# Optimization experiments

Measured on AMD Instinct MI355X. Metric: run time of the kernel, lower is better.

Reference implementation:

```python
import jax, jax.numpy as jnp
import numpy as np

N = 100000
E = 1600000
G = 64  # number of graphs
H = 128
BN_EPS = 1e-5


def setup_inputs() -> dict:
    key = jax.random.key(0)
    ks = jax.random.split(key, 12)
    x = jax.random.normal(ks[0], (N, 3), dtype=jnp.float32)
    edge_index = jax.random.randint(ks[1], (2, E), 0, N, dtype=jnp.int64)
    batch = jnp.sort(jax.random.randint(ks[2], (N,), 0, G, dtype=jnp.int64))
    W1 = jax.random.normal(ks[3], (3, H), dtype=jnp.float32) * 0.3
    W2 = jax.random.normal(ks[4], (H, H), dtype=jnp.float32) * 0.05
    W3 = jax.random.normal(ks[5], (H, H), dtype=jnp.float32) * 0.05
    lin_W = jax.random.normal(ks[6], (H, 2), dtype=jnp.float32) * 0.05
    d = {
        'x': x, 'edge_index': edge_index, 'batch': batch,
        'W1': W1, 'b1': jnp.zeros((H,), jnp.float32),
        'W2': W2, 'b2': jnp.zeros((H,), jnp.float32),
        'W3': W3, 'b3': jnp.zeros((H,), jnp.float32),
        'lin_W': lin_W, 'lin_b': jnp.zeros((2,), jnp.float32),
    }
    for i, kk in zip((1, 2, 3), ks[7:10]):
        d[f'bn{i}_g'] = jnp.ones((H,), jnp.float32)
        d[f'bn{i}_b'] = jnp.zeros((H,), jnp.float32)
        d[f'bn{i}_m'] = jnp.zeros((H,), jnp.float32)
        d[f'bn{i}_v'] = jax.random.uniform(kk, (H,), dtype=jnp.float32, minval=0.5, maxval=1.5)
    return d


def _gcn(x, src, dst, norm, W, b):
    # GCNConv: out = scatter_add(norm * (xW)[src], dst) + b
    h = x @ W
    msg = h[src] * norm[:, None]
    agg = jax.ops.segment_sum(msg, dst, num_segments=N)
    return agg + b


def _bn_eval(x, g, b, m, v):
    return (x - m) * jax.lax.rsqrt(v + BN_EPS) * g + b


def reference(x, edge_index, batch, W1, b1, W2, b2, W3, b3,
              bn1_g, bn1_b, bn1_m, bn1_v,
              bn2_g, bn2_b, bn2_m, bn2_v,
              bn3_g, bn3_b, bn3_m, bn3_v,
              lin_W, lin_b):
    loop = jnp.arange(N, dtype=edge_index.dtype)
    src = jnp.concatenate([edge_index[0], loop])
    dst = jnp.concatenate([edge_index[1], loop])
    # symmetric normalization with self-loops: deg from destination nodes
    deg = jax.ops.segment_sum(jnp.ones_like(dst, dtype=x.dtype), dst, num_segments=N)
    dinv = jnp.where(deg > 0, jax.lax.rsqrt(deg), 0.0)
    norm = dinv[src] * dinv[dst]

    h = jax.nn.relu(_bn_eval(_gcn(x, src, dst, norm, W1, b1), bn1_g, bn1_b, bn1_m, bn1_v))
    h = jax.nn.relu(_bn_eval(_gcn(h, src, dst, norm, W2, b2), bn2_g, bn2_b, bn2_m, bn2_v))
    h = jax.nn.relu(_bn_eval(_gcn(h, src, dst, norm, W3, b3), bn3_g, bn3_b, bn3_m, bn3_v))
    # dropout is identity in eval mode
    sums = jax.ops.segment_sum(h, batch, num_segments=G)
    cnts = jax.ops.segment_sum(jnp.ones((N,), h.dtype), batch, num_segments=G)
    pooled = sums / jnp.maximum(cnts, 1.0)[:, None]
    return pooled @ lin_W + lin_b
```

## Files before the change

kernel.cpp:

```cpp
#include <hip/hip_runtime.h>

#define NN 100000
#define EE 1600000
#define GG 64
#define HH 128
#define BN_EPS 1e-5f

#define CB 782
#define NB 256
#define TILE 6250

typedef unsigned short ushort_t;

static __device__ inline ushort_t f2bf(float f) {
    unsigned u = __float_as_uint(f);
    unsigned r = (u + 0x7FFF + ((u >> 16) & 1)) >> 16;
    return (ushort_t)r;
}
static __device__ inline float bf2f(ushort_t b) {
    return __uint_as_float(((unsigned)b) << 16);
}


__global__ __launch_bounds__(256) void k_hist(const int* __restrict__ ei,
                                              int* __restrict__ histG) {
    __shared__ int h[CB];
    int t = threadIdx.x;
    for (int i = t; i < CB; i += 256) h[i] = 0;
    __syncthreads();
    int e0 = blockIdx.x * TILE;
    for (int i = t; i < TILE; i += 256) {
        int d = ei[EE + e0 + i];
        atomicAdd(&h[d >> 7], 1);
    }
    __syncthreads();
    for (int i = t; i < CB; i += 256) histG[blockIdx.x * CB + i] = h[i];
}

__global__ __launch_bounds__(NB) void k_bscan(int* __restrict__ histG,
                                              int* __restrict__ total) {
    __shared__ int sh[NB];
    int t = threadIdx.x;
    int c = blockIdx.x;
    sh[t] = histG[t * CB + c];
    __syncthreads();
    for (int d = 1; d < NB; d <<= 1) {
        int x = (t >= d) ? sh[t - d] : 0;
        __syncthreads();
        sh[t] += x;
        __syncthreads();
    }
    histG[t * CB + c] = (t > 0) ? sh[t - 1] : 0;
    if (t == NB - 1) total[c] = sh[NB - 1];
}

__global__ __launch_bounds__(1024) void k_cbase(const int* __restrict__ total,
                                                int* __restrict__ cbase) {
    __shared__ int sh[1024];
    int t = threadIdx.x;
    sh[t] = (t < CB) ? total[t] : 0;
    __syncthreads();
    for (int d = 1; d < 1024; d <<= 1) {
        int x = (t >= d) ? sh[t - d] : 0;
        __syncthreads();
        sh[t] += x;
        __syncthreads();
    }
    if (t < CB) cbase[t] = (t > 0) ? sh[t - 1] : 0;
    if (t == CB - 1) cbase[CB] = sh[t];
}

__global__ __launch_bounds__(256) void k_cscatter(const int* __restrict__ ei,
                                                  const int* __restrict__ histG,
                                                  const int* __restrict__ cbase,
                                                  int* __restrict__ metaS) {
    __shared__ int base_l[CB];
    __shared__ int cur_l[CB];
    int t = threadIdx.x;
    int b = blockIdx.x;
    for (int i = t; i < CB; i += 256) {
        base_l[i] = cbase[i] + histG[b * CB + i];
        cur_l[i] = 0;
    }
    __syncthreads();
    int e0 = b * TILE;
    for (int i = t; i < TILE; i += 256) {
        int s = ei[e0 + i];
        int d = ei[EE + e0 + i];
        int c = d >> 7;
        int p = base_l[c] + atomicAdd(&cur_l[c], 1);
        metaS[p] = s | ((d & 127) << 17);
    }
}

__global__ __launch_bounds__(256) void k_fine(const int* __restrict__ metaS,
                                              const int* __restrict__ cbase,
                                              int* __restrict__ cnt,
                                              int* __restrict__ offs,
                                              int* __restrict__ col,
                                              float* __restrict__ dinv) {
    __shared__ int hist[128];
    __shared__ int scn[128];
    __shared__ int cur[128];
    int t = threadIdx.x;
    int c = blockIdx.x;
    int lo = cbase[c], hi = cbase[c + 1];
    if (t < 128) hist[t] = 0;
    __syncthreads();
    for (int r = lo + t; r < hi; r += 256) atomicAdd(&hist[metaS[r] >> 17], 1);
    __syncthreads();
    if (t < 128) scn[t] = hist[t];
    __syncthreads();
    for (int d = 1; d < 128; d <<= 1) {
        int x = (t >= d && t < 128) ? scn[t - d] : 0;
        __syncthreads();
        if (t < 128) scn[t] += x;
        __syncthreads();
    }
    if (t < 128) {
        int excl = (t > 0) ? scn[t - 1] : 0;
        cur[t] = excl;
        int node = c * 128 + t;
        if (node < NN) {
            cnt[node] = hist[t];
            offs[node] = lo + excl;
            dinv[node] = rsqrtf((float)(hist[t] + 1));
        }
    }
    __syncthreads();
    for (int r = lo + t; r < hi; r += 256) {
        int pk = metaS[r];
        int s = pk & 0x1FFFF;
        int idx = atomicAdd(&cur[pk >> 17], 1);
        col[lo + idx] = s;
    }
}


__global__ __launch_bounds__(256) void k_aggx(const float* __restrict__ x,
                                              const int* __restrict__ offs,
                                              const int* __restrict__ cnt,
                                              const int* __restrict__ col,
                                              const float* __restrict__ dinv,
                                              float* __restrict__ wgt,
                                              float4* __restrict__ agg) {
    int tid = threadIdx.x;
    int wave = tid >> 6;
    int lane = tid & 63;
    int grp = lane >> 4;
    int l = lane & 15;
    int n = blockIdx.x * 16 + wave * 4 + grp;
    float dv = dinv[n];
    int base = offs[n], cn = cnt[n];
    float a0 = 0.f, a1 = 0.f, a2 = 0.f;
    for (int i = l; i < cn; i += 16) {
        int s = col[base + i];
        float w = dinv[s] * dv;
        wgt[base + i] = w;
        a0 += w * x[s * 3 + 0];
        a1 += w * x[s * 3 + 1];
        a2 += w * x[s * 3 + 2];
    }
#pragma unroll
    for (int off = 8; off >= 1; off >>= 1) {
        a0 += __shfl_xor(a0, off, 16);
        a1 += __shfl_xor(a1, off, 16);
        a2 += __shfl_xor(a2, off, 16);
    }
    if (l == 0) {
        float w0 = dv * dv;
        a0 += w0 * x[n * 3 + 0];
        a1 += w0 * x[n * 3 + 1];
        a2 += w0 * x[n * 3 + 2];
        agg[n] = make_float4(a0, a1, a2, 0.f);
    }
}


__global__ __launch_bounds__(256) void k_mml1(const float4* __restrict__ agg,
                                              const float* __restrict__ W1,
                                              const float* __restrict__ b1,
                                              const float* __restrict__ g1,
                                              const float* __restrict__ bb1,
                                              const float* __restrict__ m1,
                                              const float* __restrict__ v1,
                                              const float* __restrict__ W2,
                                              ushort_t* __restrict__ outB) {
    __shared__ float xs[64][132];
    __shared__ float4 ag[64];
    int tid = threadIdx.x;
    int row0 = blockIdx.x * 64;
    if (tid < 64) {
        int gr = row0 + tid;
        ag[tid] = (gr < NN) ? agg[gr] : make_float4(0.f, 0.f, 0.f, 0.f);
    }
    __syncthreads();
    {
        int c = tid & 127;
        int rh = tid >> 7;
        float w0 = W1[c], w1 = W1[128 + c], w2 = W1[256 + c];
        float sc = g1[c] * rsqrtf(v1[c] + BN_EPS);
        float sh = (b1[c] - m1[c]) * sc + bb1[c];
#pragma unroll
        for (int i = 0; i < 32; i++) {
            int r = 2 * i + rh;
            float4 a = ag[r];
            float t = a.x * w0 + a.y * w1 + a.z * w2;
            xs[r][c] = fmaxf(t * sc + sh, 0.f);
        }
    }
    __syncthreads();

    int tx = tid & 31;
    int ty = tid >> 5;
    float acc[8][4];
#pragma unroll
    for (int i = 0; i < 8; i++)
#pragma unroll
        for (int j = 0; j < 4; j++) acc[i][j] = 0.f;

    const float* Wp = W2 + tx * 4;
#pragma unroll 4
    for (int k = 0; k < 128; k++) {
        float4 w = *(const float4*)&Wp[k * HH];
#pragma unroll
        for (int i = 0; i < 8; i++) {
            float xv = xs[ty * 8 + i][k];
            acc[i][0] += xv * w.x;
            acc[i][1] += xv * w.y;
            acc[i][2] += xv * w.z;
            acc[i][3] += xv * w.w;
        }
    }
#pragma unroll
    for (int i = 0; i < 8; i++) {
        int gr = row0 + ty * 8 + i;
        if (gr < NN) {
            ushort4 o;
            o.x = f2bf(acc[i][0]);
            o.y = f2bf(acc[i][1]);
            o.z = f2bf(acc[i][2]);
            o.w = f2bf(acc[i][3]);
            *(ushort4*)&outB[(size_t)gr * HH + tx * 4] = o;
        }
    }
}


__global__ __launch_bounds__(256) void k_mm(const ushort_t* __restrict__ xin,
                                            const float* __restrict__ W,
                                            ushort_t* __restrict__ outB) {
    __shared__ float xs[64][132];
    int tid = threadIdx.x;
    int tx = tid & 31;
    int ty = tid >> 5;
    int row0 = blockIdx.x * 64;
#pragma unroll
    for (int i = 0; i < 4; i++) {
        int idx8 = i * 256 + tid;
        int r = idx8 >> 4;
        int k8 = (idx8 & 15) * 8;
        int gr = row0 + r;
        int4 pk = (gr < NN) ? *(const int4*)&xin[(size_t)gr * HH + k8]
                            : make_int4(0, 0, 0, 0);
        float* dst = &xs[r][k8];
        dst[0] = __uint_as_float(((unsigned)pk.x) << 16);
        dst[1] = __uint_as_float(((unsigned)pk.x) & 0xFFFF0000u);
        dst[2] = __uint_as_float(((unsigned)pk.y) << 16);
        dst[3] = __uint_as_float(((unsigned)pk.y) & 0xFFFF0000u);
        dst[4] = __uint_as_float(((unsigned)pk.z) << 16);
        dst[5] = __uint_as_float(((unsigned)pk.z) & 0xFFFF0000u);
        dst[6] = __uint_as_float(((unsigned)pk.w) << 16);
        dst[7] = __uint_as_float(((unsigned)pk.w) & 0xFFFF0000u);
    }
    __syncthreads();
    float acc[8][4];
#pragma unroll
    for (int i = 0; i < 8; i++)
#pragma unroll
        for (int j = 0; j < 4; j++) acc[i][j] = 0.f;

    const float* Wp = W + tx * 4;
#pragma unroll 4
    for (int k = 0; k < 128; k++) {
        float4 w = *(const float4*)&Wp[k * HH];
#pragma unroll
        for (int i = 0; i < 8; i++) {
            float xv = xs[ty * 8 + i][k];
            acc[i][0] += xv * w.x;
            acc[i][1] += xv * w.y;
            acc[i][2] += xv * w.z;
            acc[i][3] += xv * w.w;
        }
    }
#pragma unroll
    for (int i = 0; i < 8; i++) {
        int gr = row0 + ty * 8 + i;
        if (gr < NN) {
            ushort4 o;
            o.x = f2bf(acc[i][0]);
            o.y = f2bf(acc[i][1]);
            o.z = f2bf(acc[i][2]);
            o.w = f2bf(acc[i][3]);
            *(ushort4*)&outB[(size_t)gr * HH + tx * 4] = o;
        }
    }
}


__global__ __launch_bounds__(256) void k_agg(const ushort_t* __restrict__ t,
                                             const int* __restrict__ offs,
                                             const int* __restrict__ cnt,
                                             const int* __restrict__ col,
                                             const float* __restrict__ wgt,
                                             const float* __restrict__ dinv,
                                             const float* __restrict__ bias,
                                             const float* __restrict__ g,
                                             const float* __restrict__ bb,
                                             const float* __restrict__ m,
                                             const float* __restrict__ v,
                                             ushort_t* __restrict__ out) {
    int wave = threadIdx.x >> 6;
    int lane = threadIdx.x & 63;
    int half = lane >> 5;
    int l = lane & 31;
    int d = blockIdx.x * 8 + wave * 2 + half;
    int c0 = l * 4;
    float dv = dinv[d];
    float w0 = dv * dv;
    ushort4 selfR = *(const ushort4*)&t[(size_t)d * HH + c0];
    float4 acc;
    acc.x = bf2f(selfR.x) * w0; acc.y = bf2f(selfR.y) * w0;
    acc.z = bf2f(selfR.z) * w0; acc.w = bf2f(selfR.w) * w0;
    int base = offs[d], cn = cnt[d];
    for (int ib = 0; ib < cn; ib += 32) {
        int i = ib + l;
        int s = 0;
        float w = 0.f;
        if (i < cn) {
            s = col[base + i];
            w = wgt[base + i];
        }
        int lim = min(32, cn - ib);
#pragma unroll 8
        for (int j = 0; j < lim; j++) {
            int ss = __shfl(s, j, 32);
            float ww = __shfl(w, j, 32);
            ushort4 tv = *(const ushort4*)&t[(size_t)ss * HH + c0];
            acc.x += ww * bf2f(tv.x);
            acc.y += ww * bf2f(tv.y);
            acc.z += ww * bf2f(tv.z);
            acc.w += ww * bf2f(tv.w);
        }
    }
    float4 gg = *(const float4*)&g[c0];
    float4 vv = *(const float4*)&v[c0];
    float4 mm = *(const float4*)&m[c0];
    float4 bv = *(const float4*)&bb[c0];
    float4 bi = *(const float4*)&bias[c0];
    float sc0 = gg.x * rsqrtf(vv.x + BN_EPS);
    float sc1 = gg.y * rsqrtf(vv.y + BN_EPS);
    float sc2 = gg.z * rsqrtf(vv.z + BN_EPS);
    float sc3 = gg.w * rsqrtf(vv.w + BN_EPS);
    ushort4 o;
    o.x = f2bf(fmaxf(acc.x * sc0 + (bi.x - mm.x) * sc0 + bv.x, 0.f));
    o.y = f2bf(fmaxf(acc.y * sc1 + (bi.y - mm.y) * sc1 + bv.y, 0.f));
    o.z = f2bf(fmaxf(acc.z * sc2 + (bi.z - mm.z) * sc2 + bv.z, 0.f));
    o.w = f2bf(fmaxf(acc.w * sc3 + (bi.w - mm.w) * sc3 + bv.w, 0.f));
    *(ushort4*)&out[(size_t)d * HH + c0] = o;
}


#define PBLK 2048
__global__ void k_pool(const ushort_t* __restrict__ h, const int* __restrict__ batch,
                       float* __restrict__ gsum, int* __restrict__ gcnt) {
    int c = threadIdx.x;
    int per = (NN + PBLK - 1) / PBLK;
    int n0 = blockIdx.x * per;
    int n1 = min(NN, n0 + per);
    if (n0 >= NN) return;
    float acc = 0.f;
    int cur = batch[n0];
    int count = 0;
    for (int n = n0; n < n1; n++) {
        int gr = batch[n];
        if (gr != cur) {
            atomicAdd(&gsum[cur * HH + c], acc);
            if (c == 0) atomicAdd(&gcnt[cur], count);
            acc = 0.f; count = 0; cur = gr;
        }
        acc += bf2f(h[(size_t)n * HH + c]);
        count++;
    }
    atomicAdd(&gsum[cur * HH + c], acc);
    if (c == 0) atomicAdd(&gcnt[cur], count);
}

__global__ void k_head(const float* __restrict__ gsum, const int* __restrict__ gcnt,
                       const float* __restrict__ linW, const float* __restrict__ linb,
                       float* __restrict__ out) {
    int t = threadIdx.x;
    int gr = t >> 1, j = t & 1;
    float inv = 1.0f / fmaxf((float)gcnt[gr], 1.0f);
    float acc = 0.f;
    for (int c = 0; c < HH; c++) acc += gsum[gr * HH + c] * linW[c * 2 + j];
    out[t] = acc * inv + linb[j];
}


static inline size_t al256(size_t x) { return (x + 255) & ~(size_t)255; }

extern "C" void kernel_launch(void* const* d_in, const int* in_sizes, int n_in,
                              void* d_out, int out_size, void* d_ws, size_t ws_size,
                              hipStream_t stream) {
    const float* x    = (const float*)d_in[0];
    const int*   ei   = (const int*)d_in[1];
    const int*   batch= (const int*)d_in[2];
    const float* W1   = (const float*)d_in[3];
    const float* b1   = (const float*)d_in[4];
    const float* W2   = (const float*)d_in[5];
    const float* b2   = (const float*)d_in[6];
    const float* W3   = (const float*)d_in[7];
    const float* b3   = (const float*)d_in[8];
    const float* linW = (const float*)d_in[9];
    const float* linb = (const float*)d_in[10];
    const float* bn1g = (const float*)d_in[11];
    const float* bn1b = (const float*)d_in[12];
    const float* bn1m = (const float*)d_in[13];
    const float* bn1v = (const float*)d_in[14];
    const float* bn2g = (const float*)d_in[15];
    const float* bn2b = (const float*)d_in[16];
    const float* bn2m = (const float*)d_in[17];
    const float* bn2v = (const float*)d_in[18];
    const float* bn3g = (const float*)d_in[19];
    const float* bn3b = (const float*)d_in[20];
    const float* bn3m = (const float*)d_in[21];
    const float* bn3v = (const float*)d_in[22];
    float* out = (float*)d_out;

    char* ws = (char*)d_ws;
    size_t off = 0;
    int*    histG  = (int*)(ws + off);    off += al256((size_t)NB * CB * 4);
    int*    total  = (int*)(ws + off);    off += al256((size_t)CB * 4);
    int*    cbase  = (int*)(ws + off);    off += al256((size_t)(CB + 1) * 4);
    int*    cnt    = (int*)(ws + off);    off += al256((size_t)NN * 4);
    int*    offs   = (int*)(ws + off);    off += al256((size_t)NN * 4);
    float*  dinv   = (float*)(ws + off);  off += al256((size_t)NN * 4);
    int*    col    = (int*)(ws + off);    off += al256((size_t)EE * 4);
    float*  wgt    = (float*)(ws + off);  off += al256((size_t)EE * 4);
    float4* agg    = (float4*)(ws + off); off += al256((size_t)NN * 16);
    char*   bufA   = (char*)(ws + off);   off += al256((size_t)NN * HH * 2);
    char*   bufB   = (char*)(ws + off);   off += al256((size_t)NN * HH * 4);
    float*  gsum   = (float*)(ws + off);  off += (size_t)GG * HH * 4;
    int*    gcnt   = (int*)(ws + off);    off += al256((size_t)GG * 4);

    int* metaS = (int*)bufB;
    ushort_t* tB = (ushort_t*)bufB;
    ushort_t* hB = (ushort_t*)bufA;

    hipMemsetAsync(gsum, 0, (size_t)GG * HH * 4 + (size_t)GG * 4, stream);

    k_hist<<<NB, 256, 0, stream>>>(ei, histG);
    k_bscan<<<CB, NB, 0, stream>>>(histG, total);
    k_cbase<<<1, 1024, 0, stream>>>(total, cbase);
    k_cscatter<<<NB, 256, 0, stream>>>(ei, histG, cbase, metaS);
    k_fine<<<CB, 256, 0, stream>>>(metaS, cbase, cnt, offs, col, dinv);

    k_aggx<<<NN / 16, 256, 0, stream>>>(x, offs, cnt, col, dinv, wgt, agg);

    k_mml1<<<(NN + 63) / 64, 256, 0, stream>>>(agg, W1, b1, bn1g, bn1b, bn1m, bn1v,
                                               W2, tB);
    k_agg<<<NN / 8, 256, 0, stream>>>(tB, offs, cnt, col, wgt, dinv,
                                      b2, bn2g, bn2b, bn2m, bn2v, hB);

    k_mm<<<(NN + 63) / 64, 256, 0, stream>>>(hB, W3, tB);
    k_agg<<<NN / 8, 256, 0, stream>>>(tB, offs, cnt, col, wgt, dinv,
                                      b3, bn3g, bn3b, bn3m, bn3v, hB);

    k_pool<<<PBLK, 128, 0, stream>>>(hB, batch, gsum, gcnt);
    k_head<<<1, 128, 0, stream>>>(gsum, gcnt, linW, linb, out);
}
```

Measured before the change: 442.8 us.

## Fuse GCN aggregation with following matmul and pooling into per-tile kernels

Merges the layer-1 x aggregation into the first matmul kernel, fuses layer-2 aggregation+BN+ReLU with the layer-3 matmul through shared memory, and fuses layer-3 aggregation with mean pooling. The per-edge weight array is no longer stored; weights are recomputed from dinv on the fly. This removes intermediate bf16 activation round-trips to global memory and several kernel launches. The cost is lower parallelism per block (64 nodes per block, fewer blocks) and a larger block size for the fused aggregation kernels.

```diff
diff --git a/kernel.cpp b/kernel.cpp
--- a/kernel.cpp
+++ b/kernel.cpp
@@ -137,62 +137,55 @@
 }
 
 
-__global__ __launch_bounds__(256) void k_aggx(const float* __restrict__ x,
-                                              const int* __restrict__ offs,
-                                              const int* __restrict__ cnt,
-                                              const int* __restrict__ col,
-                                              const float* __restrict__ dinv,
-                                              float* __restrict__ wgt,
-                                              float4* __restrict__ agg) {
-    int tid = threadIdx.x;
-    int wave = tid >> 6;
-    int lane = tid & 63;
-    int grp = lane >> 4;
-    int l = lane & 15;
-    int n = blockIdx.x * 16 + wave * 4 + grp;
-    float dv = dinv[n];
-    int base = offs[n], cn = cnt[n];
-    float a0 = 0.f, a1 = 0.f, a2 = 0.f;
-    for (int i = l; i < cn; i += 16) {
-        int s = col[base + i];
-        float w = dinv[s] * dv;
-        wgt[base + i] = w;
-        a0 += w * x[s * 3 + 0];
-        a1 += w * x[s * 3 + 1];
-        a2 += w * x[s * 3 + 2];
-    }
-#pragma unroll
-    for (int off = 8; off >= 1; off >>= 1) {
-        a0 += __shfl_xor(a0, off, 16);
-        a1 += __shfl_xor(a1, off, 16);
-        a2 += __shfl_xor(a2, off, 16);
-    }
-    if (l == 0) {
-        float w0 = dv * dv;
-        a0 += w0 * x[n * 3 + 0];
-        a1 += w0 * x[n * 3 + 1];
-        a2 += w0 * x[n * 3 + 2];
-        agg[n] = make_float4(a0, a1, a2, 0.f);
-    }
-}
-
-
-__global__ __launch_bounds__(256) void k_mml1(const float4* __restrict__ agg,
-                                              const float* __restrict__ W1,
-                                              const float* __restrict__ b1,
-                                              const float* __restrict__ g1,
-                                              const float* __restrict__ bb1,
-                                              const float* __restrict__ m1,
-                                              const float* __restrict__ v1,
-                                              const float* __restrict__ W2,
-                                              ushort_t* __restrict__ outB) {
+__global__ __launch_bounds__(256) void k_l12(const float* __restrict__ x,
+                                             const int* __restrict__ offs,
+                                             const int* __restrict__ cnt,
+                                             const int* __restrict__ col,
+                                             const float* __restrict__ dinv,
+                                             const float* __restrict__ W1,
+                                             const float* __restrict__ b1,
+                                             const float* __restrict__ g1,
+                                             const float* __restrict__ bb1,
+                                             const float* __restrict__ m1,
+                                             const float* __restrict__ v1,
+                                             const float* __restrict__ W2,
+                                             ushort_t* __restrict__ outB) {
     __shared__ float xs[64][132];
     __shared__ float4 ag[64];
     int tid = threadIdx.x;
     int row0 = blockIdx.x * 64;
-    if (tid < 64) {
-        int gr = row0 + tid;
-        ag[tid] = (gr < NN) ? agg[gr] : make_float4(0.f, 0.f, 0.f, 0.f);
+    int hw = tid >> 5;
+    int l = tid & 31;
+    for (int k = 0; k < 8; k++) {
+        int r = hw * 8 + k;
+        int d = row0 + r;
+        float a0 = 0.f, a1 = 0.f, a2 = 0.f;
+        if (d < NN) {
+            float dv = dinv[d];
+            int base = offs[d], cn2 = cnt[d];
+            for (int i = l; i < cn2; i += 32) {
+                int s = col[base + i];
+                float w = dinv[s] * dv;
+                a0 += w * x[s * 3 + 0];
+                a1 += w * x[s * 3 + 1];
+                a2 += w * x[s * 3 + 2];
+            }
+#pragma unroll
+            for (int off = 16; off >= 1; off >>= 1) {
+                a0 += __shfl_xor(a0, off, 32);
+                a1 += __shfl_xor(a1, off, 32);
+                a2 += __shfl_xor(a2, off, 32);
+            }
+            if (l == 0) {
+                float w0 = dv * dv;
+                a0 += w0 * x[d * 3 + 0];
+                a1 += w0 * x[d * 3 + 1];
+                a2 += w0 * x[d * 3 + 2];
+                ag[r] = make_float4(a0, a1, a2, 0.f);
+            }
+        } else if (l == 0) {
+            ag[r] = make_float4(0.f, 0.f, 0.f, 0.f);
+        }
     }
     __syncthreads();
     {
@@ -210,7 +203,6 @@
         }
     }
     __syncthreads();
-
     int tx = tid & 31;
     int ty = tid >> 5;
     float acc[8][4];
@@ -218,7 +210,6 @@
     for (int i = 0; i < 8; i++)
 #pragma unroll
         for (int j = 0; j < 4; j++) acc[i][j] = 0.f;
-
     const float* Wp = W2 + tx * 4;
 #pragma unroll 4
     for (int k = 0; k < 128; k++) {
@@ -247,112 +238,24 @@
 }
 
 
-__global__ __launch_bounds__(256) void k_mm(const ushort_t* __restrict__ xin,
-                                            const float* __restrict__ W,
-                                            ushort_t* __restrict__ outB) {
+__global__ __launch_bounds__(512) void k_aggmm(const ushort_t* __restrict__ t,
+                                               const int* __restrict__ offs,
+                                               const int* __restrict__ cnt,
+                                               const int* __restrict__ col,
+                                               const float* __restrict__ dinv,
+                                               const float* __restrict__ bias,
+                                               const float* __restrict__ g,
+                                               const float* __restrict__ bb,
+                                               const float* __restrict__ m,
+                                               const float* __restrict__ v,
+                                               const float* __restrict__ W3,
+                                               ushort_t* __restrict__ outB) {
     __shared__ float xs[64][132];
     int tid = threadIdx.x;
-    int tx = tid & 31;
-    int ty = tid >> 5;
     int row0 = blockIdx.x * 64;
-#pragma unroll
-    for (int i = 0; i < 4; i++) {
-        int idx8 = i * 256 + tid;
-        int r = idx8 >> 4;
-        int k8 = (idx8 & 15) * 8;
-        int gr = row0 + r;
-        int4 pk = (gr < NN) ? *(const int4*)&xin[(size_t)gr * HH + k8]
-                            : make_int4(0, 0, 0, 0);
-        float* dst = &xs[r][k8];
-        dst[0] = __uint_as_float(((unsigned)pk.x) << 16);
-        dst[1] = __uint_as_float(((unsigned)pk.x) & 0xFFFF0000u);
-        dst[2] = __uint_as_float(((unsigned)pk.y) << 16);
-        dst[3] = __uint_as_float(((unsigned)pk.y) & 0xFFFF0000u);
-        dst[4] = __uint_as_float(((unsigned)pk.z) << 16);
-        dst[5] = __uint_as_float(((unsigned)pk.z) & 0xFFFF0000u);
-        dst[6] = __uint_as_float(((unsigned)pk.w) << 16);
-        dst[7] = __uint_as_float(((unsigned)pk.w) & 0xFFFF0000u);
-    }
-    __syncthreads();
-    float acc[8][4];
-#pragma unroll
-    for (int i = 0; i < 8; i++)
-#pragma unroll
-        for (int j = 0; j < 4; j++) acc[i][j] = 0.f;
-
-    const float* Wp = W + tx * 4;
-#pragma unroll 4
-    for (int k = 0; k < 128; k++) {
-        float4 w = *(const float4*)&Wp[k * HH];
-#pragma unroll
-        for (int i = 0; i < 8; i++) {
-            float xv = xs[ty * 8 + i][k];
-            acc[i][0] += xv * w.x;
-            acc[i][1] += xv * w.y;
-            acc[i][2] += xv * w.z;
-            acc[i][3] += xv * w.w;
-        }
-    }
-#pragma unroll
-    for (int i = 0; i < 8; i++) {
-        int gr = row0 + ty * 8 + i;
-        if (gr < NN) {
-            ushort4 o;
-            o.x = f2bf(acc[i][0]);
-            o.y = f2bf(acc[i][1]);
-            o.z = f2bf(acc[i][2]);
-            o.w = f2bf(acc[i][3]);
-            *(ushort4*)&outB[(size_t)gr * HH + tx * 4] = o;
-        }
-    }
-}
-
-
-__global__ __launch_bounds__(256) void k_agg(const ushort_t* __restrict__ t,
-                                             const int* __restrict__ offs,
-                                             const int* __restrict__ cnt,
-                                             const int* __restrict__ col,
-                                             const float* __restrict__ wgt,
-                                             const float* __restrict__ dinv,
-                                             const float* __restrict__ bias,
-                                             const float* __restrict__ g,
-                                             const float* __restrict__ bb,
-                                             const float* __restrict__ m,
-                                             const float* __restrict__ v,
-                                             ushort_t* __restrict__ out) {
-    int wave = threadIdx.x >> 6;
-    int lane = threadIdx.x & 63;
-    int half = lane >> 5;
-    int l = lane & 31;
-    int d = blockIdx.x * 8 + wave * 2 + half;
+    int hw = tid >> 5;
+    int l = tid & 31;
     int c0 = l * 4;
-    float dv = dinv[d];
-    float w0 = dv * dv;
-    ushort4 selfR = *(const ushort4*)&t[(size_t)d * HH + c0];
-    float4 acc;
-    acc.x = bf2f(selfR.x) * w0; acc.y = bf2f(selfR.y) * w0;
-    acc.z = bf2f(selfR.z) * w0; acc.w = bf2f(selfR.w) * w0;
-    int base = offs[d], cn = cnt[d];
-    for (int ib = 0; ib < cn; ib += 32) {
-        int i = ib + l;
-        int s = 0;
-        float w = 0.f;
-        if (i < cn) {
-            s = col[base + i];
-            w = wgt[base + i];
-        }
-        int lim = min(32, cn - ib);
-#pragma unroll 8
-        for (int j = 0; j < lim; j++) {
-            int ss = __shfl(s, j, 32);
-            float ww = __shfl(w, j, 32);
-            ushort4 tv = *(const ushort4*)&t[(size_t)ss * HH + c0];
-            acc.x += ww * bf2f(tv.x);
-            acc.y += ww * bf2f(tv.y);
-            acc.z += ww * bf2f(tv.z);
-            acc.w += ww * bf2f(tv.w);
-        }
-    }
     float4 gg = *(const float4*)&g[c0];
     float4 vv = *(const float4*)&v[c0];
     float4 mm = *(const float4*)&m[c0];
@@ -362,38 +265,190 @@
     float sc1 = gg.y * rsqrtf(vv.y + BN_EPS);
     float sc2 = gg.z * rsqrtf(vv.z + BN_EPS);
     float sc3 = gg.w * rsqrtf(vv.w + BN_EPS);
-    ushort4 o;
-    o.x = f2bf(fmaxf(acc.x * sc0 + (bi.x - mm.x) * sc0 + bv.x, 0.f));
-    o.y = f2bf(fmaxf(acc.y * sc1 + (bi.y - mm.y) * sc1 + bv.y, 0.f));
-    o.z = f2bf(fmaxf(acc.z * sc2 + (bi.z - mm.z) * sc2 + bv.z, 0.f));
-    o.w = f2bf(fmaxf(acc.w * sc3 + (bi.w - mm.w) * sc3 + bv.w, 0.f));
-    *(ushort4*)&out[(size_t)d * HH + c0] = o;
-}
-
-
-#define PBLK 2048
-__global__ void k_pool(const ushort_t* __restrict__ h, const int* __restrict__ batch,
-                       float* __restrict__ gsum, int* __restrict__ gcnt) {
-    int c = threadIdx.x;
-    int per = (NN + PBLK - 1) / PBLK;
-    int n0 = blockIdx.x * per;
-    int n1 = min(NN, n0 + per);
-    if (n0 >= NN) return;
-    float acc = 0.f;
-    int cur = batch[n0];
-    int count = 0;
-    for (int n = n0; n < n1; n++) {
-        int gr = batch[n];
-        if (gr != cur) {
-            atomicAdd(&gsum[cur * HH + c], acc);
-            if (c == 0) atomicAdd(&gcnt[cur], count);
-            acc = 0.f; count = 0; cur = gr;
-        }
-        acc += bf2f(h[(size_t)n * HH + c]);
-        count++;
-    }
-    atomicAdd(&gsum[cur * HH + c], acc);
-    if (c == 0) atomicAdd(&gcnt[cur], count);
+    float sh0 = (bi.x - mm.x) * sc0 + bv.x;
+    float sh1 = (bi.y - mm.y) * sc1 + bv.y;
+    float sh2 = (bi.z - mm.z) * sc2 + bv.z;
+    float sh3 = (bi.w - mm.w) * sc3 + bv.w;
+    for (int k = 0; k < 4; k++) {
+        int r = hw * 4 + k;
+        int d = row0 + r;
+        float4 o = make_float4(0.f, 0.f, 0.f, 0.f);
+        if (d < NN) {
+            float dv = dinv[d];
+            float w0 = dv * dv;
+            ushort4 selfR = *(const ushort4*)&t[(size_t)d * HH + c0];
+            float4 acc;
+            acc.x = bf2f(selfR.x) * w0; acc.y = bf2f(selfR.y) * w0;
+            acc.z = bf2f(selfR.z) * w0; acc.w = bf2f(selfR.w) * w0;
+            int base = offs[d], cn2 = cnt[d];
+            for (int ib = 0; ib < cn2; ib += 32) {
+                int i = ib + l;
+                int s = 0;
+                float w = 0.f;
+                if (i < cn2) {
+                    s = col[base + i];
+                    w = dinv[s] * dv;
+                }
+                int lim = min(32, cn2 - ib);
+#pragma unroll 8
+                for (int j = 0; j < lim; j++) {
+                    int ss = __shfl(s, j, 32);
+                    float ww = __shfl(w, j, 32);
+                    ushort4 tv = *(const ushort4*)&t[(size_t)ss * HH + c0];
+                    acc.x += ww * bf2f(tv.x);
+                    acc.y += ww * bf2f(tv.y);
+                    acc.z += ww * bf2f(tv.z);
+                    acc.w += ww * bf2f(tv.w);
+                }
+            }
+            o.x = fmaxf(acc.x * sc0 + sh0, 0.f);
+            o.y = fmaxf(acc.y * sc1 + sh1, 0.f);
+            o.z = fmaxf(acc.z * sc2 + sh2, 0.f);
+            o.w = fmaxf(acc.w * sc3 + sh3, 0.f);
+        }
+        *(float4*)&xs[r][c0] = o;
+    }
+    __syncthreads();
+    int tx = tid & 31;
+    int ty = tid >> 5;
+    float acc2[4][4];
+#pragma unroll
+    for (int i = 0; i < 4; i++)
+#pragma unroll
+        for (int j = 0; j < 4; j++) acc2[i][j] = 0.f;
+    const float* Wp = W3 + tx * 4;
+#pragma unroll 4
+    for (int k = 0; k < 128; k++) {
+        float4 w = *(const float4*)&Wp[k * HH];
+#pragma unroll
+        for (int i = 0; i < 4; i++) {
+            float xv = xs[ty * 4 + i][k];
+            acc2[i][0] += xv * w.x;
+            acc2[i][1] += xv * w.y;
+            acc2[i][2] += xv * w.z;
+            acc2[i][3] += xv * w.w;
+        }
+    }
+#pragma unroll
+    for (int i = 0; i < 4; i++) {
+        int gr = row0 + ty * 4 + i;
+        if (gr < NN) {
+            ushort4 o;
+            o.x = f2bf(acc2[i][0]);
+            o.y = f2bf(acc2[i][1]);
+            o.z = f2bf(acc2[i][2]);
+            o.w = f2bf(acc2[i][3]);
+            *(ushort4*)&outB[(size_t)gr * HH + tx * 4] = o;
+        }
+    }
+}
+
+
+__global__ __launch_bounds__(512) void k_aggpool(const ushort_t* __restrict__ t,
+                                                 const int* __restrict__ offs,
+                                                 const int* __restrict__ cnt,
+                                                 const int* __restrict__ col,
+                                                 const float* __restrict__ dinv,
+                                                 const float* __restrict__ bias,
+                                                 const float* __restrict__ g,
+                                                 const float* __restrict__ bb,
+                                                 const float* __restrict__ m,
+                                                 const float* __restrict__ v,
+                                                 const int* __restrict__ batch,
+                                                 float* __restrict__ gsum,
+                                                 int* __restrict__ gcnt) {
+    __shared__ float xs[64][132];
+    __shared__ int bsh[64];
+    int tid = threadIdx.x;
+    int row0 = blockIdx.x * 64;
+    int hw = tid >> 5;
+    int l = tid & 31;
+    int c0 = l * 4;
+    float4 gg = *(const float4*)&g[c0];
+    float4 vv = *(const float4*)&v[c0];
+    float4 mm = *(const float4*)&m[c0];
+    float4 bv = *(const float4*)&bb[c0];
+    float4 bi = *(const float4*)&bias[c0];
+    float sc0 = gg.x * rsqrtf(vv.x + BN_EPS);
+    float sc1 = gg.y * rsqrtf(vv.y + BN_EPS);
+    float sc2 = gg.z * rsqrtf(vv.z + BN_EPS);
+    float sc3 = gg.w * rsqrtf(vv.w + BN_EPS);
+    float sh0 = (bi.x - mm.x) * sc0 + bv.x;
+    float sh1 = (bi.y - mm.y) * sc1 + bv.y;
+    float sh2 = (bi.z - mm.z) * sc2 + bv.z;
+    float sh3 = (bi.w - mm.w) * sc3 + bv.w;
+    if (tid < 64) {
+        int n = row0 + tid;
+        bsh[tid] = (n < NN) ? batch[n] : -1;
+    }
+    for (int k = 0; k < 4; k++) {
+        int r = hw * 4 + k;
+        int d = row0 + r;
+        float4 o = make_float4(0.f, 0.f, 0.f, 0.f);
+        if (d < NN) {
+            float dv = dinv[d];
+            float w0 = dv * dv;
+            ushort4 selfR = *(const ushort4*)&t[(size_t)d * HH + c0];
+            float4 acc;
+            acc.x = bf2f(selfR.x) * w0; acc.y = bf2f(selfR.y) * w0;
+            acc.z = bf2f(selfR.z) * w0; acc.w = bf2f(selfR.w) * w0;
+            int base = offs[d], cn2 = cnt[d];
+            for (int ib = 0; ib < cn2; ib += 32) {
+                int i = ib + l;
+                int s = 0;
+                float w = 0.f;
+                if (i < cn2) {
+                    s = col[base + i];
+                    w = dinv[s] * dv;
+                }
+                int lim = min(32, cn2 - ib);
+#pragma unroll 8
+                for (int j = 0; j < lim; j++) {
+                    int ss = __shfl(s, j, 32);
+                    float ww = __shfl(w, j, 32);
+                    ushort4 tv = *(const ushort4*)&t[(size_t)ss * HH + c0];
+                    acc.x += ww * bf2f(tv.x);
+                    acc.y += ww * bf2f(tv.y);
+                    acc.z += ww * bf2f(tv.z);
+                    acc.w += ww * bf2f(tv.w);
+                }
+            }
+            o.x = fmaxf(acc.x * sc0 + sh0, 0.f);
+            o.y = fmaxf(acc.y * sc1 + sh1, 0.f);
+            o.z = fmaxf(acc.z * sc2 + sh2, 0.f);
+            o.w = fmaxf(acc.w * sc3 + sh3, 0.f);
+        }
+        *(float4*)&xs[r][c0] = o;
+    }
+    __syncthreads();
+    if (tid < 128) {
+        int c = tid;
+        float acc = 0.f;
+        int cur = bsh[0];
+        for (int r = 0; r < 64; r++) {
+            int gr2 = bsh[r];
+            if (gr2 < 0) break;
+            if (gr2 != cur) {
+                atomicAdd(&gsum[cur * HH + c], acc);
+                acc = 0.f; cur = gr2;
+            }
+            acc += xs[r][c];
+        }
+        atomicAdd(&gsum[cur * HH + c], acc);
+    } else if (tid == 128) {
+        int cur = bsh[0];
+        int count = 0;
+        for (int r = 0; r < 64; r++) {
+            int gr2 = bsh[r];
+            if (gr2 < 0) break;
+            if (gr2 != cur) {
+                atomicAdd(&gcnt[cur], count);
+                count = 0; cur = gr2;
+            }
+            count++;
+        }
+        atomicAdd(&gcnt[cur], count);
+    }
 }
 
 __global__ void k_head(const float* __restrict__ gsum, const int* __restrict__ gcnt,
@@ -447,16 +502,14 @@
     int*    offs   = (int*)(ws + off);    off += al256((size_t)NN * 4);
     float*  dinv   = (float*)(ws + off);  off += al256((size_t)NN * 4);
     int*    col    = (int*)(ws + off);    off += al256((size_t)EE * 4);
-    float*  wgt    = (float*)(ws + off);  off += al256((size_t)EE * 4);
-    float4* agg    = (float4*)(ws + off); off += al256((size_t)NN * 16);
-    char*   bufA   = (char*)(ws + off);   off += al256((size_t)NN * HH * 2);
-    char*   bufB   = (char*)(ws + off);   off += al256((size_t)NN * HH * 4);
+    char*   buf2   = (char*)(ws + off);   off += al256((size_t)NN * HH * 2);
+    char*   buf3   = (char*)(ws + off);   off += al256((size_t)NN * HH * 2);
     float*  gsum   = (float*)(ws + off);  off += (size_t)GG * HH * 4;
     int*    gcnt   = (int*)(ws + off);    off += al256((size_t)GG * 4);
 
-    int* metaS = (int*)bufB;
-    ushort_t* tB = (ushort_t*)bufB;
-    ushort_t* hB = (ushort_t*)bufA;
+    int* metaS = (int*)buf2;
+    ushort_t* t2 = (ushort_t*)buf2;
+    ushort_t* t3 = (ushort_t*)buf3;
 
     hipMemsetAsync(gsum, 0, (size_t)GG * HH * 4 + (size_t)GG * 4, stream);
 
@@ -466,17 +519,17 @@
     k_cscatter<<<NB, 256, 0, stream>>>(ei, histG, cbase, metaS);
     k_fine<<<CB, 256, 0, stream>>>(metaS, cbase, cnt, offs, col, dinv);
 
-    k_aggx<<<NN / 16, 256, 0, stream>>>(x, offs, cnt, col, dinv, wgt, agg);
-
-    k_mml1<<<(NN + 63) / 64, 256, 0, stream>>>(agg, W1, b1, bn1g, bn1b, bn1m, bn1v,
-                                               W2, tB);
-    k_agg<<<NN / 8, 256, 0, stream>>>(tB, offs, cnt, col, wgt, dinv,
-                                      b2, bn2g, bn2b, bn2m, bn2v, hB);
-
-    k_mm<<<(NN + 63) / 64, 256, 0, stream>>>(hB, W3, tB);
-    k_agg<<<NN / 8, 256, 0, stream>>>(tB, offs, cnt, col, wgt, dinv,
-                                      b3, bn3g, bn3b, bn3m, bn3v, hB);
-
-    k_pool<<<PBLK, 128, 0, stream>>>(hB, batch, gsum, gcnt);
+    int nblk64 = (NN + 63) / 64;
+
+    k_l12<<<nblk64, 256, 0, stream>>>(x, offs, cnt, col, dinv,
+                                      W1, b1, bn1g, bn1b, bn1m, bn1v, W2, t2);
+
+    k_aggmm<<<nblk64, 512, 0, stream>>>(t2, offs, cnt, col, dinv,
+                                        b2, bn2g, bn2b, bn2m, bn2v, W3, t3);
+
+    k_aggpool<<<nblk64, 512, 0, stream>>>(t3, offs, cnt, col, dinv,
+                                          b3, bn3g, bn3b, bn3m, bn3v,
+                                          batch, gsum, gcnt);
+
     k_head<<<1, 128, 0, stream>>>(gsum, gcnt, linW, linb, out);
 }
```

Measured after the change: 448.7 us. No clear change (+1.3%).

## Slice-major feature layout, fuse layer-1 gather into matmul, fuse pooling into last aggregation

Applied to the files above, without the earlier changes.

Stores the bf16 hidden features in a slice-major layout (8 slices of 16 channels per node), so each aggregation block gathers neighbor rows from a single 3.2 MB slice and gets better cache locality. The layer-1 neighbor gather is folded into the first matmul kernel. Edge weights are recomputed from dinv on the fly, so the wgt array is gone, and the final aggregation now accumulates mean-pool sums directly. The costs are 8x more blocks, each reading the column indices again, fewer bytes per gather, and more atomics into gsum.

```diff
diff --git a/kernel.cpp b/kernel.cpp
--- a/kernel.cpp
+++ b/kernel.cpp
@@ -137,62 +137,55 @@
 }
 
 
-__global__ __launch_bounds__(256) void k_aggx(const float* __restrict__ x,
-                                              const int* __restrict__ offs,
-                                              const int* __restrict__ cnt,
-                                              const int* __restrict__ col,
-                                              const float* __restrict__ dinv,
-                                              float* __restrict__ wgt,
-                                              float4* __restrict__ agg) {
-    int tid = threadIdx.x;
-    int wave = tid >> 6;
-    int lane = tid & 63;
-    int grp = lane >> 4;
-    int l = lane & 15;
-    int n = blockIdx.x * 16 + wave * 4 + grp;
-    float dv = dinv[n];
-    int base = offs[n], cn = cnt[n];
-    float a0 = 0.f, a1 = 0.f, a2 = 0.f;
-    for (int i = l; i < cn; i += 16) {
-        int s = col[base + i];
-        float w = dinv[s] * dv;
-        wgt[base + i] = w;
-        a0 += w * x[s * 3 + 0];
-        a1 += w * x[s * 3 + 1];
-        a2 += w * x[s * 3 + 2];
-    }
-#pragma unroll
-    for (int off = 8; off >= 1; off >>= 1) {
-        a0 += __shfl_xor(a0, off, 16);
-        a1 += __shfl_xor(a1, off, 16);
-        a2 += __shfl_xor(a2, off, 16);
-    }
-    if (l == 0) {
-        float w0 = dv * dv;
-        a0 += w0 * x[n * 3 + 0];
-        a1 += w0 * x[n * 3 + 1];
-        a2 += w0 * x[n * 3 + 2];
-        agg[n] = make_float4(a0, a1, a2, 0.f);
-    }
-}
-
-
-__global__ __launch_bounds__(256) void k_mml1(const float4* __restrict__ agg,
-                                              const float* __restrict__ W1,
-                                              const float* __restrict__ b1,
-                                              const float* __restrict__ g1,
-                                              const float* __restrict__ bb1,
-                                              const float* __restrict__ m1,
-                                              const float* __restrict__ v1,
-                                              const float* __restrict__ W2,
-                                              ushort_t* __restrict__ outB) {
+__global__ __launch_bounds__(256) void k_l12(const float* __restrict__ x,
+                                             const int* __restrict__ offs,
+                                             const int* __restrict__ cnt,
+                                             const int* __restrict__ col,
+                                             const float* __restrict__ dinv,
+                                             const float* __restrict__ W1,
+                                             const float* __restrict__ b1,
+                                             const float* __restrict__ g1,
+                                             const float* __restrict__ bb1,
+                                             const float* __restrict__ m1,
+                                             const float* __restrict__ v1,
+                                             const float* __restrict__ W2,
+                                             ushort_t* __restrict__ outB) {
     __shared__ float xs[64][132];
     __shared__ float4 ag[64];
     int tid = threadIdx.x;
     int row0 = blockIdx.x * 64;
-    if (tid < 64) {
-        int gr = row0 + tid;
-        ag[tid] = (gr < NN) ? agg[gr] : make_float4(0.f, 0.f, 0.f, 0.f);
+    int hw = tid >> 5;
+    int l = tid & 31;
+    for (int k = 0; k < 8; k++) {
+        int r = hw * 8 + k;
+        int d = row0 + r;
+        float a0 = 0.f, a1 = 0.f, a2 = 0.f;
+        if (d < NN) {
+            float dv = dinv[d];
+            int base = offs[d], cn2 = cnt[d];
+            for (int i = l; i < cn2; i += 32) {
+                int s = col[base + i];
+                float w = dinv[s] * dv;
+                a0 += w * x[s * 3 + 0];
+                a1 += w * x[s * 3 + 1];
+                a2 += w * x[s * 3 + 2];
+            }
+#pragma unroll
+            for (int off = 16; off >= 1; off >>= 1) {
+                a0 += __shfl_xor(a0, off, 32);
+                a1 += __shfl_xor(a1, off, 32);
+                a2 += __shfl_xor(a2, off, 32);
+            }
+            if (l == 0) {
+                float w0 = dv * dv;
+                a0 += w0 * x[d * 3 + 0];
+                a1 += w0 * x[d * 3 + 1];
+                a2 += w0 * x[d * 3 + 2];
+                ag[r] = make_float4(a0, a1, a2, 0.f);
+            }
+        } else if (l == 0) {
+            ag[r] = make_float4(0.f, 0.f, 0.f, 0.f);
+        }
     }
     __syncthreads();
     {
@@ -210,7 +203,6 @@
         }
     }
     __syncthreads();
-
     int tx = tid & 31;
     int ty = tid >> 5;
     float acc[8][4];
@@ -218,7 +210,6 @@
     for (int i = 0; i < 8; i++)
 #pragma unroll
         for (int j = 0; j < 4; j++) acc[i][j] = 0.f;
-
     const float* Wp = W2 + tx * 4;
 #pragma unroll 4
     for (int k = 0; k < 128; k++) {
@@ -232,6 +223,7 @@
             acc[i][3] += xv * w.w;
         }
     }
+    int c0 = tx * 4;
 #pragma unroll
     for (int i = 0; i < 8; i++) {
         int gr = row0 + ty * 8 + i;
@@ -241,9 +233,69 @@
             o.y = f2bf(acc[i][1]);
             o.z = f2bf(acc[i][2]);
             o.w = f2bf(acc[i][3]);
-            *(ushort4*)&outB[(size_t)gr * HH + tx * 4] = o;
-        }
-    }
+            size_t addr = ((size_t)(c0 >> 4) * NN + gr) * 16 + (c0 & 15);
+            *(ushort4*)&outB[addr] = o;
+        }
+    }
+}
+
+
+__global__ __launch_bounds__(256) void k_aggs(const ushort_t* __restrict__ t,
+                                              const int* __restrict__ offs,
+                                              const int* __restrict__ cnt,
+                                              const int* __restrict__ col,
+                                              const float* __restrict__ dinv,
+                                              const float* __restrict__ bias,
+                                              const float* __restrict__ g,
+                                              const float* __restrict__ bb,
+                                              const float* __restrict__ m,
+                                              const float* __restrict__ v,
+                                              ushort_t* __restrict__ outS) {
+    int slice = blockIdx.x & 7;
+    int chunk = blockIdx.x >> 3;
+    int tid = threadIdx.x;
+    int lane = tid & 63;
+    int wave = tid >> 6;
+    int grp = lane >> 3;
+    int l = lane & 7;
+    int r = wave * 8 + grp;
+    int d = chunk * 32 + r;
+    int c = slice * 16 + l * 2;
+    const ushort_t* tS = t + (size_t)slice * NN * 16;
+    float dvd = dinv[d];
+    float w00 = dvd * dvd;
+    unsigned su = *(const unsigned*)&tS[(size_t)d * 16 + l * 2];
+    float a0 = bf2f((ushort_t)(su & 0xFFFF)) * w00;
+    float a1 = bf2f((ushort_t)(su >> 16)) * w00;
+    int base = offs[d], cn2 = cnt[d];
+    int lb = lane & ~7;
+    for (int ib = 0; ib < cn2; ib += 16) {
+        int iA = ib + l, iB = ib + 8 + l;
+        int pkA = (iA < cn2) ? __builtin_nontemporal_load(&col[base + iA]) : 0;
+        int pkB = (iB < cn2) ? __builtin_nontemporal_load(&col[base + iB]) : 0;
+        float wA = dinv[pkA] * dvd;
+        float wB = dinv[pkB] * dvd;
+        int lim = min(16, cn2 - ib);
+#pragma unroll 4
+        for (int j = 0; j < lim; j++) {
+            int src = (j < 8) ? __shfl(pkA, lb + j) : __shfl(pkB, lb + j - 8);
+            float ww = (j < 8) ? __shfl(wA, lb + j) : __shfl(wB, lb + j - 8);
+            unsigned tv = *(const unsigned*)&tS[(size_t)src * 16 + l * 2];
+            a0 += ww * bf2f((ushort_t)(tv & 0xFFFF));
+            a1 += ww * bf2f((ushort_t)(tv >> 16));
+        }
+    }
+    float2 gg = *(const float2*)&g[c];
+    float2 vv = *(const float2*)&v[c];
+    float2 mm = *(const float2*)&m[c];
+    float2 bv = *(const float2*)&bb[c];
+    float2 bi = *(const float2*)&bias[c];
+    float sc0 = gg.x * rsqrtf(vv.x + BN_EPS);
+    float sc1 = gg.y * rsqrtf(vv.y + BN_EPS);
+    float o0 = fmaxf(a0 * sc0 + (bi.x - mm.x) * sc0 + bv.x, 0.f);
+    float o1 = fmaxf(a1 * sc1 + (bi.y - mm.y) * sc1 + bv.y, 0.f);
+    unsigned ow = ((unsigned)f2bf(o1) << 16) | (unsigned)f2bf(o0);
+    *(unsigned*)&outS[((size_t)slice * NN + d) * 16 + l * 2] = ow;
 }
 
 
@@ -261,8 +313,8 @@
         int r = idx8 >> 4;
         int k8 = (idx8 & 15) * 8;
         int gr = row0 + r;
-        int4 pk = (gr < NN) ? *(const int4*)&xin[(size_t)gr * HH + k8]
-                            : make_int4(0, 0, 0, 0);
+        size_t addr = ((size_t)(k8 >> 4) * NN + gr) * 16 + (k8 & 15);
+        int4 pk = (gr < NN) ? *(const int4*)&xin[addr] : make_int4(0, 0, 0, 0);
         float* dst = &xs[r][k8];
         dst[0] = __uint_as_float(((unsigned)pk.x) << 16);
         dst[1] = __uint_as_float(((unsigned)pk.x) & 0xFFFF0000u);
@@ -293,6 +345,7 @@
             acc[i][3] += xv * w.w;
         }
     }
+    int c0 = tx * 4;
 #pragma unroll
     for (int i = 0; i < 8; i++) {
         int gr = row0 + ty * 8 + i;
@@ -302,98 +355,99 @@
             o.y = f2bf(acc[i][1]);
             o.z = f2bf(acc[i][2]);
             o.w = f2bf(acc[i][3]);
-            *(ushort4*)&outB[(size_t)gr * HH + tx * 4] = o;
-        }
-    }
-}
-
-
-__global__ __launch_bounds__(256) void k_agg(const ushort_t* __restrict__ t,
-                                             const int* __restrict__ offs,
-                                             const int* __restrict__ cnt,
-                                             const int* __restrict__ col,
-                                             const float* __restrict__ wgt,
-                                             const float* __restrict__ dinv,
-                                             const float* __restrict__ bias,
-                                             const float* __restrict__ g,
-                                             const float* __restrict__ bb,
-                                             const float* __restrict__ m,
-                                             const float* __restrict__ v,
-                                             ushort_t* __restrict__ out) {
-    int wave = threadIdx.x >> 6;
-    int lane = threadIdx.x & 63;
-    int half = lane >> 5;
-    int l = lane & 31;
-    int d = blockIdx.x * 8 + wave * 2 + half;
-    int c0 = l * 4;
-    float dv = dinv[d];
-    float w0 = dv * dv;
-    ushort4 selfR = *(const ushort4*)&t[(size_t)d * HH + c0];
-    float4 acc;
-    acc.x = bf2f(selfR.x) * w0; acc.y = bf2f(selfR.y) * w0;
-    acc.z = bf2f(selfR.z) * w0; acc.w = bf2f(selfR.w) * w0;
-    int base = offs[d], cn = cnt[d];
-    for (int ib = 0; ib < cn; ib += 32) {
-        int i = ib + l;
-        int s = 0;
-        float w = 0.f;
-        if (i < cn) {
-            s = col[base + i];
-            w = wgt[base + i];
-        }
-        int lim = min(32, cn - ib);
-#pragma unroll 8
+            size_t addr = ((size_t)(c0 >> 4) * NN + gr) * 16 + (c0 & 15);
+            *(ushort4*)&outB[addr] = o;
+        }
+    }
+}
+
+
+__global__ __launch_bounds__(256) void k_aggspool(const ushort_t* __restrict__ t,
+                                                  const int* __restrict__ offs,
+                                                  const int* __restrict__ cnt,
+                                                  const int* __restrict__ col,
+                                                  const float* __restrict__ dinv,
+                                                  const float* __restrict__ bias,
+                                                  const float* __restrict__ g,
+                                                  const float* __restrict__ bb,
+                                                  const float* __restrict__ m,
+                                                  const float* __restrict__ v,
+                                                  const int* __restrict__ batch,
+                                                  float* __restrict__ gsum,
+                                                  int* __restrict__ gcnt) {
+    __shared__ float sh[32][16];
+    __shared__ int bsh[32];
+    int slice = blockIdx.x & 7;
+    int chunk = blockIdx.x >> 3;
+    int tid = threadIdx.x;
+    int lane = tid & 63;
+    int wave = tid >> 6;
+    int grp = lane >> 3;
+    int l = lane & 7;
+    int r = wave * 8 + grp;
+    int d = chunk * 32 + r;
+    int c = slice * 16 + l * 2;
+    if (tid < 32) bsh[tid] = batch[chunk * 32 + tid];
+    const ushort_t* tS = t + (size_t)slice * NN * 16;
+    float dvd = dinv[d];
+    float w00 = dvd * dvd;
+    unsigned su = *(const unsigned*)&tS[(size_t)d * 16 + l * 2];
+    float a0 = bf2f((ushort_t)(su & 0xFFFF)) * w00;
+    float a1 = bf2f((ushort_t)(su >> 16)) * w00;
+    int base = offs[d], cn2 = cnt[d];
+    int lb = lane & ~7;
+    for (int ib = 0; ib < cn2; ib += 16) {
+        int iA = ib + l, iB = ib + 8 + l;
+        int pkA = (iA < cn2) ? __builtin_nontemporal_load(&col[base + iA]) : 0;
+        int pkB = (iB < cn2) ? __builtin_nontemporal_load(&col[base + iB]) : 0;
+        float wA = dinv[pkA] * dvd;
+        float wB = dinv[pkB] * dvd;
+        int lim = min(16, cn2 - ib);
+#pragma unroll 4
         for (int j = 0; j < lim; j++) {
-            int ss = __shfl(s, j, 32);
-            float ww = __shfl(w, j, 32);
-            ushort4 tv = *(const ushort4*)&t[(size_t)ss * HH + c0];
-            acc.x += ww * bf2f(tv.x);
-            acc.y += ww * bf2f(tv.y);
-            acc.z += ww * bf2f(tv.z);
-            acc.w += ww * bf2f(tv.w);
-        }
-    }
-    float4 gg = *(const float4*)&g[c0];
-    float4 vv = *(const float4*)&v[c0];
-    float4 mm = *(const float4*)&m[c0];
-    float4 bv = *(const float4*)&bb[c0];
-    float4 bi = *(const float4*)&bias[c0];
+            int src = (j < 8) ? __shfl(pkA, lb + j) : __shfl(pkB, lb + j - 8);
+            float ww = (j < 8) ? __shfl(wA, lb + j) : __shfl(wB, lb + j - 8);
+            unsigned tv = *(const unsigned*)&tS[(size_t)src * 16 + l * 2];
+            a0 += ww * bf2f((ushort_t)(tv & 0xFFFF));
+            a1 += ww * bf2f((ushort_t)(tv >> 16));
+        }
+    }
+    float2 gg = *(const float2*)&g[c];
+    float2 vv = *(const float2*)&v[c];
+    float2 mm = *(const float2*)&m[c];
+    float2 bv = *(const float2*)&bb[c];
+    float2 bi = *(const float2*)&bias[c];
     float sc0 = gg.x * rsqrtf(vv.x + BN_EPS);
     float sc1 = gg.y * rsqrtf(vv.y + BN_EPS);
-    float sc2 = gg.z * rsqrtf(vv.z + BN_EPS);
-    float sc3 = gg.w * rsqrtf(vv.w + BN_EPS);
-    ushort4 o;
-    o.x = f2bf(fmaxf(acc.x * sc0 + (bi.x - mm.x) * sc0 + bv.x, 0.f));
-    o.y = f2bf(fmaxf(acc.y * sc1 + (bi.y - mm.y) * sc1 + bv.y, 0.f));
-    o.z = f2bf(fmaxf(acc.z * sc2 + (bi.z - mm.z) * sc2 + bv.z, 0.f));
-    o.w = f2bf(fmaxf(acc.w * sc3 + (bi.w - mm.w) * sc3 + bv.w, 0.f));
-    *(ushort4*)&out[(size_t)d * HH + c0] = o;
-}
-
-
-#define PBLK 2048
-__global__ void k_pool(const ushort_t* __restrict__ h, const int* __restrict__ batch,
-                       float* __restrict__ gsum, int* __restrict__ gcnt) {
-    int c = threadIdx.x;
-    int per = (NN + PBLK - 1) / PBLK;
-    int n0 = blockIdx.x * per;
-    int n1 = min(NN, n0 + per);
-    if (n0 >= NN) return;
-    float acc = 0.f;
-    int cur = batch[n0];
-    int count = 0;
-    for (int n = n0; n < n1; n++) {
-        int gr = batch[n];
-        if (gr != cur) {
-            atomicAdd(&gsum[cur * HH + c], acc);
-            if (c == 0) atomicAdd(&gcnt[cur], count);
-            acc = 0.f; count = 0; cur = gr;
-        }
-        acc += bf2f(h[(size_t)n * HH + c]);
-        count++;
-    }
-    atomicAdd(&gsum[cur * HH + c], acc);
-    if (c == 0) atomicAdd(&gcnt[cur], count);
+    sh[r][l * 2 + 0] = fmaxf(a0 * sc0 + (bi.x - mm.x) * sc0 + bv.x, 0.f);
+    sh[r][l * 2 + 1] = fmaxf(a1 * sc1 + (bi.y - mm.y) * sc1 + bv.y, 0.f);
+    __syncthreads();
+    if (tid < 16) {
+        int cc = tid;
+        float acc = 0.f;
+        int cur = bsh[0];
+        for (int rr = 0; rr < 32; rr++) {
+            int g2 = bsh[rr];
+            if (g2 != cur) {
+                atomicAdd(&gsum[cur * HH + slice * 16 + cc], acc);
+                acc = 0.f; cur = g2;
+            }
+            acc += sh[rr][cc];
+        }
+        atomicAdd(&gsum[cur * HH + slice * 16 + cc], acc);
+    } else if (tid == 16 && slice == 0) {
+        int cur = bsh[0];
+        int count = 0;
+        for (int rr = 0; rr < 32; rr++) {
+            int g2 = bsh[rr];
+            if (g2 != cur) {
+                atomicAdd(&gcnt[cur], count);
+                count = 0; cur = g2;
+            }
+            count++;
+        }
+        atomicAdd(&gcnt[cur], count);
+    }
 }
 
 __global__ void k_head(const float* __restrict__ gsum, const int* __restrict__ gcnt,
@@ -446,17 +500,15 @@
     int*    cnt    = (int*)(ws + off);    off += al256((size_t)NN * 4);
     int*    offs   = (int*)(ws + off);    off += al256((size_t)NN * 4);
     float*  dinv   = (float*)(ws + off);  off += al256((size_t)NN * 4);
-    int*    col    = (int*)(ws + off);    off += al256((size_t)EE * 4);
-    float*  wgt    = (float*)(ws + off);  off += al256((size_t)EE * 4);
-    float4* agg    = (float4*)(ws + off); off += al256((size_t)NN * 16);
-    char*   bufA   = (char*)(ws + off);   off += al256((size_t)NN * HH * 2);
-    char*   bufB   = (char*)(ws + off);   off += al256((size_t)NN * HH * 4);
+    int*    col    = (int*)(ws + off);    off += al256((size_t)(EE + 64) * 4);
+    char*   buf2   = (char*)(ws + off);   off += al256((size_t)NN * HH * 2);
+    char*   buf3   = (char*)(ws + off);   off += al256((size_t)NN * HH * 2);
     float*  gsum   = (float*)(ws + off);  off += (size_t)GG * HH * 4;
     int*    gcnt   = (int*)(ws + off);    off += al256((size_t)GG * 4);
 
-    int* metaS = (int*)bufB;
-    ushort_t* tB = (ushort_t*)bufB;
-    ushort_t* hB = (ushort_t*)bufA;
+    int* metaS = (int*)buf2;
+    ushort_t* t2 = (ushort_t*)buf2;
+    ushort_t* t3 = (ushort_t*)buf3;
 
     hipMemsetAsync(gsum, 0, (size_t)GG * HH * 4 + (size_t)GG * 4, stream);
 
@@ -466,17 +518,20 @@
     k_cscatter<<<NB, 256, 0, stream>>>(ei, histG, cbase, metaS);
     k_fine<<<CB, 256, 0, stream>>>(metaS, cbase, cnt, offs, col, dinv);
 
-    k_aggx<<<NN / 16, 256, 0, stream>>>(x, offs, cnt, col, dinv, wgt, agg);
-
-    k_mml1<<<(NN + 63) / 64, 256, 0, stream>>>(agg, W1, b1, bn1g, bn1b, bn1m, bn1v,
-                                               W2, tB);
-    k_agg<<<NN / 8, 256, 0, stream>>>(tB, offs, cnt, col, wgt, dinv,
-                                      b2, bn2g, bn2b, bn2m, bn2v, hB);
-
-    k_mm<<<(NN + 63) / 64, 256, 0, stream>>>(hB, W3, tB);
-    k_agg<<<NN / 8, 256, 0, stream>>>(tB, offs, cnt, col, wgt, dinv,
-                                      b3, bn3g, bn3b, bn3m, bn3v, hB);
-
-    k_pool<<<PBLK, 128, 0, stream>>>(hB, batch, gsum, gcnt);
+    int nblk64 = (NN + 63) / 64;
+    int nblkS  = (NN / 32) * 8;
+
+    k_l12<<<nblk64, 256, 0, stream>>>(x, offs, cnt, col, dinv,
+                                      W1, b1, bn1g, bn1b, bn1m, bn1v, W2, t2);
+
+    k_aggs<<<nblkS, 256, 0, stream>>>(t2, offs, cnt, col, dinv,
+                                      b2, bn2g, bn2b, bn2m, bn2v, (ushort_t*)buf3);
+
+    k_mm<<<nblk64, 256, 0, stream>>>((const ushort_t*)buf3, W3, t2);
+
+    k_aggspool<<<nblkS, 256, 0, stream>>>(t2, offs, cnt, col, dinv,
+                                          b3, bn3g, bn3b, bn3m, bn3v,
+                                          batch, gsum, gcnt);
+
     k_head<<<1, 128, 0, stream>>>(gsum, gcnt, linW, linb, out);
 }
```

After: 666.8 us. +50.6%, slower.
